# Performance work log

Hardware: AMD Instinct MI355X
Metric: run time of the kernel (lower is better)

## Reference

```python
import jax, jax.numpy as jnp
import numpy as np

N_NODES = 100000
N_EDGES = 1600000
N_GRAPHS = 2048
BN_EPS = 1e-5


def _bn(h, gamma, beta):
    # BatchNorm1d in training mode: biased batch stats over the node axis
    mean = jnp.mean(h, axis=0)
    var = jnp.var(h, axis=0)
    return gamma * (h - mean) * jax.lax.rsqrt(var + BN_EPS) + beta


def _gin_layer(x, src, dst, w1, b1, gamma, beta, w2, b2):
    # GINConv with eps=0: mlp(x + sum_{j->i} x_j)
    agg = jax.ops.segment_sum(x[src], dst, num_segments=N_NODES)
    h = agg + x
    h = h @ w1 + b1
    h = jax.nn.relu(_bn(h, gamma, beta))
    h = h @ w2 + b2
    return jax.nn.relu(h)  # outer F.relu after GINConv (dropout = identity in eval)


def setup_inputs() -> dict:
    key = jax.random.key(0)
    ks = jax.random.split(key, 24)
    d = {}
    d['x'] = jax.random.normal(ks[0], (N_NODES, 66), dtype=jnp.float32)
    d['edge_index'] = jax.random.randint(ks[1], (2, N_EDGES), 0, N_NODES, dtype=jnp.int64)
    d['batch'] = jnp.sort(jax.random.randint(ks[2], (N_NODES,), 0, N_GRAPHS, dtype=jnp.int64))
    dims = [(66, 128), (128, 256), (256, 128)]
    ki = 3
    for li, (din, dout) in enumerate(dims):
        s1 = 1.0 / np.sqrt(din)
        s2 = 1.0 / np.sqrt(dout)
        d[f'g{li}_w1'] = jax.random.uniform(ks[ki + 0], (din, dout), jnp.float32, -s1, s1)
        d[f'g{li}_b1'] = jax.random.uniform(ks[ki + 1], (dout,), jnp.float32, -s1, s1)
        d[f'g{li}_gamma'] = jnp.ones((dout,), jnp.float32)
        d[f'g{li}_beta'] = jnp.zeros((dout,), jnp.float32)
        d[f'g{li}_w2'] = jax.random.uniform(ks[ki + 2], (dout, dout), jnp.float32, -s2, s2)
        d[f'g{li}_b2'] = jax.random.uniform(ks[ki + 3], (dout,), jnp.float32, -s2, s2)
        ki += 4
    fcd = [(128, 1024), (1024, 128)]
    for li, (din, dout) in enumerate(fcd):
        s = 1.0 / np.sqrt(din)
        d[f'fc{li}_w'] = jax.random.uniform(ks[ki + 0], (din, dout), jnp.float32, -s, s)
        d[f'fc{li}_b'] = jax.random.uniform(ks[ki + 1], (dout,), jnp.float32, -s, s)
        ki += 2
    return d


def reference(x, edge_index, batch,
              g0_w1, g0_b1, g0_gamma, g0_beta, g0_w2, g0_b2,
              g1_w1, g1_b1, g1_gamma, g1_beta, g1_w2, g1_b2,
              g2_w1, g2_b1, g2_gamma, g2_beta, g2_w2, g2_b2,
              fc0_w, fc0_b, fc1_w, fc1_b):
    src, dst = edge_index[0], edge_index[1]
    h = _gin_layer(x, src, dst, g0_w1, g0_b1, g0_gamma, g0_beta, g0_w2, g0_b2)
    h = _gin_layer(h, src, dst, g1_w1, g1_b1, g1_gamma, g1_beta, g1_w2, g1_b2)
    h = _gin_layer(h, src, dst, g2_w1, g2_b1, g2_gamma, g2_beta, g2_w2, g2_b2)
    # global_add_pool over graphs
    g = jax.ops.segment_sum(h, batch, num_segments=N_GRAPHS)
    g = jax.nn.relu(g @ fc0_w + fc0_b)
    return g @ fc1_w + fc1_b
```

## Files before the change

### kernel.cpp

```cpp
#include <hip/hip_runtime.h>

#define NNODES 100000
#define NEDGES 1600000
#define NGRAPHS 2048
#define BN_EPS 1e-5f

typedef __attribute__((ext_vector_type(8))) short bf16x8;
typedef __attribute__((ext_vector_type(4))) float f32x4;

__device__ __forceinline__ short f2bf(float x) {
    unsigned u = __float_as_uint(x);
    unsigned r = u + 0x7FFF + ((u >> 16) & 1);
    return (short)(r >> 16);
}
__device__ __forceinline__ float bf2f(short h) {
    return __uint_as_float(((unsigned)(unsigned short)h) << 16);
}

__global__ __launch_bounds__(256) void degoff_kernel(const int* __restrict__ dstA,
                                                     int* __restrict__ degp,
                                                     int* __restrict__ off) {
    int e = blockIdx.x * 256 + threadIdx.x;
    if (e < NEDGES) {
        int d = dstA[e];
        int c = atomicAdd(&degp[d << 4], 1);
        off[e] = (d << 8) | c;
    }
}

__global__ __launch_bounds__(256) void scan1_kernel(const int* __restrict__ degp,
                                                    int* __restrict__ partials) {
    int b = blockIdx.x;
    int i = b * 256 + threadIdx.x;
    int v = (i < NNODES) ? degp[i << 4] : 0;
    __shared__ int wsum[4];
#pragma unroll
    for (int off = 32; off; off >>= 1) v += __shfl_down(v, off);
    if ((threadIdx.x & 63) == 0) wsum[threadIdx.x >> 6] = v;
    __syncthreads();
    if (threadIdx.x == 0) partials[b] = wsum[0] + wsum[1] + wsum[2] + wsum[3];
}

__global__ __launch_bounds__(512) void scan2_kernel(int* __restrict__ partials, int nb) {
    __shared__ int s[512];
    int t = threadIdx.x;
    int v = (t < nb) ? partials[t] : 0;
    s[t] = v;
    __syncthreads();
    for (int off = 1; off < 512; off <<= 1) {
        int u = (t >= off) ? s[t - off] : 0;
        __syncthreads();
        s[t] += u;
        __syncthreads();
    }
    if (t < nb) partials[t] = s[t] - v;
}

__global__ __launch_bounds__(256) void scan3_kernel(const int* __restrict__ degp,
                                                    const int* __restrict__ partials,
                                                    int* __restrict__ rowptr,
                                                    const int* __restrict__ batch,
                                                    int* __restrict__ gstart) {
    int b = blockIdx.x;
    int t = threadIdx.x;
    int i = b * 256 + t;
    __shared__ int s[256];
    int v = (i < NNODES) ? degp[i << 4] : 0;
    s[t] = v;
    __syncthreads();
    for (int off = 1; off < 256; off <<= 1) {
        int u = (t >= off) ? s[t - off] : 0;
        __syncthreads();
        s[t] += u;
        __syncthreads();
    }
    if (i < NNODES) {
        int ex = partials[b] + s[t] - v;
        rowptr[i] = ex;
        int bb = batch[i];
        int bp = (i == 0) ? -1 : batch[i - 1];
        for (int g = bp + 1; g <= bb; ++g) gstart[g] = i;
        if (i == NNODES - 1)
            for (int g = bb + 1; g <= NGRAPHS; ++g) gstart[g] = NNODES;
    }
    if (b == 0 && t == 0) rowptr[NNODES] = NEDGES;
}

__global__ __launch_bounds__(256) void fill2_kernel(const int* __restrict__ srcA,
                                                    const int* __restrict__ rowptr,
                                                    const int* __restrict__ off,
                                                    int* __restrict__ adj) {
    int e = blockIdx.x * 256 + threadIdx.x;
    if (e < NEDGES) {
        int v = off[e];
        adj[rowptr[v >> 8] + (v & 255)] = srcA[e];
    }
}

template <int DIM, int CHUNK, int OSTRIDE, bool SPLIT>
__global__ __launch_bounds__(256) void gather_kernel(const float* __restrict__ x,
                                                     const int* __restrict__ rowptr,
                                                     const int* __restrict__ adj,
                                                     float* __restrict__ agg,
                                                     short* __restrict__ oh,
                                                     short* __restrict__ ol,
                                                     const float* __restrict__ bias) {
    constexpr int PE = DIM / CHUNK;
    constexpr int PEL = SPLIT ? (OSTRIDE / CHUNK) : PE;
    int gid = blockIdx.x * 256 + threadIdx.x;
    if (gid >= NNODES * PEL) return;
    int node = gid / PEL;
    int c = gid - node * PEL;
    if constexpr (SPLIT) {
        if (c >= PE) {
            size_t o = (size_t)node * OSTRIDE + c * CHUNK;
            if constexpr (CHUNK == 4) {
                short4 z;
                z.x = z.y = z.z = z.w = 0;
                *(short4*)&oh[o] = z;
                *(short4*)&ol[o] = z;
            } else {
                short2 z;
                z.x = z.y = 0;
                *(short2*)&oh[o] = z;
                *(short2*)&ol[o] = z;
            }
            return;
        }
    }
    const int beg = rowptr[node];
    const int end = rowptr[node + 1];
    if constexpr (CHUNK == 4) {
        const float4* xp = (const float4*)x;
        float4 acc = xp[(size_t)node * PE + c];
        float4 acc1 = make_float4(0.f, 0.f, 0.f, 0.f);
        int i = beg;
        for (; i + 4 <= end; i += 4) {
            int s0 = adj[i + 0];
            int s1 = adj[i + 1];
            int s2 = adj[i + 2];
            int s3 = adj[i + 3];
            float4 v0 = xp[(size_t)s0 * PE + c];
            float4 v1 = xp[(size_t)s1 * PE + c];
            float4 v2 = xp[(size_t)s2 * PE + c];
            float4 v3 = xp[(size_t)s3 * PE + c];
            acc.x += v0.x + v1.x;
            acc.y += v0.y + v1.y;
            acc.z += v0.z + v1.z;
            acc.w += v0.w + v1.w;
            acc1.x += v2.x + v3.x;
            acc1.y += v2.y + v3.y;
            acc1.z += v2.z + v3.z;
            acc1.w += v2.w + v3.w;
        }
        for (; i < end; ++i) {
            int s = adj[i];
            float4 v = xp[(size_t)s * PE + c];
            acc.x += v.x;
            acc.y += v.y;
            acc.z += v.z;
            acc.w += v.w;
        }
        acc.x += acc1.x;
        acc.y += acc1.y;
        acc.z += acc1.z;
        acc.w += acc1.w;
        if (bias) {
            float4 b = *(const float4*)&bias[c * 4];
            acc.x += b.x;
            acc.y += b.y;
            acc.z += b.z;
            acc.w += b.w;
        }
        if constexpr (SPLIT) {
            size_t o = (size_t)node * OSTRIDE + c * 4;
            short4 h4, l4;
            h4.x = f2bf(acc.x);
            l4.x = f2bf(acc.x - bf2f(h4.x));
            h4.y = f2bf(acc.y);
            l4.y = f2bf(acc.y - bf2f(h4.y));
            h4.z = f2bf(acc.z);
            l4.z = f2bf(acc.z - bf2f(h4.z));
            h4.w = f2bf(acc.w);
            l4.w = f2bf(acc.w - bf2f(h4.w));
            *(short4*)&oh[o] = h4;
            *(short4*)&ol[o] = l4;
        } else {
            *(float4*)&agg[(size_t)node * OSTRIDE + c * 4] = acc;
        }
    } else {
        const float2* xp = (const float2*)x;
        float2 acc = xp[(size_t)node * PE + c];
        float2 acc1 = make_float2(0.f, 0.f);
        int i = beg;
        for (; i + 4 <= end; i += 4) {
            int s0 = adj[i + 0];
            int s1 = adj[i + 1];
            int s2 = adj[i + 2];
            int s3 = adj[i + 3];
            float2 v0 = xp[(size_t)s0 * PE + c];
            float2 v1 = xp[(size_t)s1 * PE + c];
            float2 v2 = xp[(size_t)s2 * PE + c];
            float2 v3 = xp[(size_t)s3 * PE + c];
            acc.x += v0.x + v1.x;
            acc.y += v0.y + v1.y;
            acc1.x += v2.x + v3.x;
            acc1.y += v2.y + v3.y;
        }
        for (; i < end; ++i) {
            int s = adj[i];
            float2 v = xp[(size_t)s * PE + c];
            acc.x += v.x;
            acc.y += v.y;
        }
        acc.x += acc1.x;
        acc.y += acc1.y;
        if constexpr (SPLIT) {
            size_t o = (size_t)node * OSTRIDE + c * 2;
            short2 h2, l2;
            h2.x = f2bf(acc.x);
            l2.x = f2bf(acc.x - bf2f(h2.x));
            h2.y = f2bf(acc.y);
            l2.y = f2bf(acc.y - bf2f(h2.y));
            *(short2*)&oh[o] = h2;
            *(short2*)&ol[o] = l2;
        } else {
            *(float2*)&agg[(size_t)node * OSTRIDE + c * 2] = acc;
        }
    }
}

template <int N>
__global__ __launch_bounds__(256) void bnstats_kernel(const float* __restrict__ h,
                                                      float* __restrict__ sums) {
    constexpr int SHIFT = (N == 128) ? 7 : 8;
    int t = blockIdx.x * 256 + threadIdx.x;
    int col = t & (N - 1);
    int slice = t >> SHIFT;
    float s = 0.f, s2 = 0.f;
    for (int r = slice; r < NNODES; r += 256) {
        float v = h[(size_t)r * N + col];
        s += v;
        s2 += v * v;
    }
    atomicAdd(&sums[col], s);
    atomicAdd(&sums[256 + col], s2);
}

__global__ void bnfinal_kernel(float* __restrict__ sums, const float* __restrict__ gamma,
                               const float* __restrict__ beta, float* __restrict__ scsh, int N,
                               float invM) {
    int c = threadIdx.x;
    if (c < N) {
        float mean = sums[c] * invM;
        float var = sums[256 + c] * invM - mean * mean;
        float sc = gamma[c] * rsqrtf(var + BN_EPS);
        scsh[c] = sc;
        scsh[256 + c] = beta[c] - mean * sc;
    }
    sums[c] = 0.f;
    sums[256 + c] = 0.f;
}

struct WDesc {
    const float* W;
    int Kw, N, KT, hioff, looff;
};
struct WDescs {
    WDesc d[8];
    int cum[9];
};
__global__ __launch_bounds__(256) void wprep_all_kernel(WDescs wd, short* __restrict__ wf) {
    int idx = blockIdx.x * 256 + threadIdx.x;
    if (idx >= wd.cum[8]) return;
    int s = 0;
#pragma unroll
    for (int i = 1; i < 8; ++i) s += (idx >= wd.cum[i]);
    int r = idx - wd.cum[s];
    const WDesc D = wd.d[s];
    int j = r & 7;
    int lane = (r >> 3) & 63;
    int t = r >> 9;
    int kt = t % D.KT;
    int nt = t / D.KT;
    int k = kt * 32 + ((lane >> 4) << 3) + j;
    int n = (nt << 4) + (lane & 15);
    float w = (k < D.Kw) ? D.W[(size_t)k * D.N + n] : 0.f;
    short hi = f2bf(w);
    wf[D.hioff + r] = hi;
    wf[D.looff + r] = f2bf(w - bf2f(hi));
}

template <int NT, int KTLOOP, bool BNRELU_A, bool RELU_OUT, bool FUSE_STATS, bool SPLITK,
          bool ASPLIT, bool SPLIT_OUT, int MINW>
__global__ __launch_bounds__(256, MINW) void gemm_mfma_kernel(
    const float* __restrict__ A, const short* __restrict__ Ah, const short* __restrict__ Al,
    const short* __restrict__ whi, const short* __restrict__ wlo, const float* __restrict__ bias,
    const float* __restrict__ scsh, float* __restrict__ C, short* __restrict__ Ch,
    short* __restrict__ Cl, float* __restrict__ stats, int M, int Kst, int KT, int N) {
    __shared__ float sstat[512];
    const int tid = threadIdx.x;
    const int wave = tid >> 6;
    const int lane = tid & 63;
    const int quad = lane >> 4;
    const int l16 = lane & 15;
    const int mrow = blockIdx.x * 64 + wave * 16 + l16;
    const int ngrp = blockIdx.y * NT * 16;
    const size_t wgrp = (size_t)blockIdx.y * NT * KT * 512;
    const int ktbeg = SPLITK ? blockIdx.z * KTLOOP : 0;
    float* Cb = SPLITK ? C + (size_t)blockIdx.z * M * N : C;

    if (FUSE_STATS) {
        sstat[tid] = 0.f;
        sstat[tid + 256] = 0.f;
        __syncthreads();
    }

    f32x4 acc[NT] = {};

    auto kstep = [&](int kt) {
        const int kq = kt * 32 + quad * 8;
        bf16x8 ahi, alo;
        if constexpr (ASPLIT) {
            ahi = *(const bf16x8*)(Ah + (size_t)mrow * Kst + kq);
            alo = *(const bf16x8*)(Al + (size_t)mrow * Kst + kq);
        } else {
            const float* ap = A + (size_t)mrow * Kst + kq;
            float4 x0 = *(const float4*)ap;
            float4 x1 = *(const float4*)(ap + 4);
            float a8[8] = {x0.x, x0.y, x0.z, x0.w, x1.x, x1.y, x1.z, x1.w};
            if constexpr (BNRELU_A) {
                float4 sc0 = *(const float4*)&scsh[kq];
                float4 sc1 = *(const float4*)&scsh[kq + 4];
                float4 sh0 = *(const float4*)&scsh[256 + kq];
                float4 sh1 = *(const float4*)&scsh[256 + kq + 4];
                float sc[8] = {sc0.x, sc0.y, sc0.z, sc0.w, sc1.x, sc1.y, sc1.z, sc1.w};
                float sh[8] = {sh0.x, sh0.y, sh0.z, sh0.w, sh1.x, sh1.y, sh1.z, sh1.w};
#pragma unroll
                for (int i = 0; i < 8; ++i) a8[i] = fmaxf(a8[i] * sc[i] + sh[i], 0.f);
            }
#pragma unroll
            for (int i = 0; i < 8; ++i) {
                short h = f2bf(a8[i]);
                ahi[i] = h;
                alo[i] = f2bf(a8[i] - bf2f(h));
            }
        }
#pragma unroll
        for (int nt = 0; nt < NT; ++nt) {
            const size_t boff = wgrp + (((size_t)nt * KT + kt) << 9) + ((size_t)lane << 3);
            bf16x8 bh = *(const bf16x8*)(whi + boff);
            bf16x8 bl = *(const bf16x8*)(wlo + boff);
            acc[nt] = __builtin_amdgcn_mfma_f32_16x16x32_bf16(ahi, bh, acc[nt], 0, 0, 0);
            acc[nt] = __builtin_amdgcn_mfma_f32_16x16x32_bf16(alo, bh, acc[nt], 0, 0, 0);
            acc[nt] = __builtin_amdgcn_mfma_f32_16x16x32_bf16(ahi, bl, acc[nt], 0, 0, 0);
            acc[nt] = __builtin_amdgcn_mfma_f32_16x16x32_bf16(alo, bl, acc[nt], 0, 0, 0);
        }
    };

    if constexpr (ASPLIT) {
#pragma unroll 2
        for (int k = 0; k < KTLOOP; ++k) kstep(ktbeg + k);
    } else {
#pragma unroll 1
        for (int k = 0; k < KTLOOP; ++k) kstep(ktbeg + k);
    }

    const int mbase = blockIdx.x * 64 + wave * 16 + quad * 4;
#pragma unroll
    for (int nt = 0; nt < NT; ++nt) {
        int gn = ngrp + nt * 16 + l16;
        float bv = bias ? bias[gn] : 0.f;
        float s = 0.f, s2 = 0.f;
#pragma unroll
        for (int r = 0; r < 4; ++r) {
            int gm = mbase + r;
            float v = acc[nt][r] + bv;
            if (RELU_OUT) v = fmaxf(v, 0.f);
            if (gm < M) {
                if constexpr (SPLIT_OUT) {
                    short h = f2bf(v);
                    Ch[(size_t)gm * N + gn] = h;
                    Cl[(size_t)gm * N + gn] = f2bf(v - bf2f(h));
                } else {
                    Cb[(size_t)gm * N + gn] = v;
                }
                if (FUSE_STATS) {
                    s += v;
                    s2 += v * v;
                }
            }
        }
        if (FUSE_STATS) {
            s += __shfl_xor(s, 16);
            s += __shfl_xor(s, 32);
            s2 += __shfl_xor(s2, 16);
            s2 += __shfl_xor(s2, 32);
            if (quad == 0) {
                atomicAdd(&sstat[gn], s);
                atomicAdd(&sstat[256 + gn], s2);
            }
        }
    }
    if (FUSE_STATS) {
        __syncthreads();
        if (tid < N) {
            atomicAdd(&stats[tid], sstat[tid]);
            atomicAdd(&stats[256 + tid], sstat[256 + tid]);
        }
    }
}

__global__ __launch_bounds__(256) void splitk_reduce_kernel(const float* __restrict__ part,
                                                            const float* __restrict__ bias,
                                                            float* __restrict__ out) {
    const int i4 = blockIdx.x * 256 + threadIdx.x;
    const int TOT4 = NGRAPHS * 128 / 4;
    if (i4 >= TOT4) return;
    const float4* p = (const float4*)part;
    float4 acc = make_float4(0.f, 0.f, 0.f, 0.f);
#pragma unroll
    for (int c = 0; c < 8; ++c) {
        float4 v = p[(size_t)c * TOT4 + i4];
        acc.x += v.x;
        acc.y += v.y;
        acc.z += v.z;
        acc.w += v.w;
    }
    float4 b = ((const float4*)bias)[i4 & 31];
    acc.x += b.x;
    acc.y += b.y;
    acc.z += b.z;
    acc.w += b.w;
    ((float4*)out)[i4] = acc;
}

template <bool SPLIT>
__global__ __launch_bounds__(128) void pool_seg_kernel(const float* __restrict__ h,
                                                       const int* __restrict__ gstart,
                                                       float* __restrict__ g,
                                                       short* __restrict__ oh,
                                                       short* __restrict__ ol) {
    int gr = blockIdx.x;
    int t = threadIdx.x;
    int beg = gstart[gr];
    int end = gstart[gr + 1];
    float acc = 0.f;
    for (int r = beg; r < end; ++r) acc += h[(size_t)r * 128 + t];
    if constexpr (SPLIT) {
        short hh = f2bf(acc);
        oh[(size_t)gr * 128 + t] = hh;
        ol[(size_t)gr * 128 + t] = f2bf(acc - bf2f(hh));
    } else {
        g[(size_t)gr * 128 + t] = acc;
    }
}

extern "C" void kernel_launch(void* const* d_in, const int* in_sizes, int n_in, void* d_out,
                              int out_size, void* d_ws, size_t ws_size, hipStream_t stream) {
    const float* x = (const float*)d_in[0];
    const int* ei = (const int*)d_in[1];
    const int* batch = (const int*)d_in[2];
    const int* srcA = ei;
    const int* dstA = ei + NEDGES;

    const float* g0_w1 = (const float*)d_in[3];
    const float* g0_b1 = (const float*)d_in[4];
    const float* g0_ga = (const float*)d_in[5];
    const float* g0_be = (const float*)d_in[6];
    const float* g0_w2 = (const float*)d_in[7];
    const float* g0_b2 = (const float*)d_in[8];
    const float* g1_w1 = (const float*)d_in[9];
    const float* g1_b1 = (const float*)d_in[10];
    const float* g1_ga = (const float*)d_in[11];
    const float* g1_be = (const float*)d_in[12];
    const float* g1_w2 = (const float*)d_in[13];
    const float* g1_b2 = (const float*)d_in[14];
    const float* g2_w1 = (const float*)d_in[15];
    const float* g2_b1 = (const float*)d_in[16];
    const float* g2_ga = (const float*)d_in[17];
    const float* g2_be = (const float*)d_in[18];
    const float* g2_w2 = (const float*)d_in[19];
    const float* g2_b2 = (const float*)d_in[20];
    const float* fc0_w = (const float*)d_in[21];
    const float* fc0_b = (const float*)d_in[22];
    const float* fc1_w = (const float*)d_in[23];
    const float* fc1_b = (const float*)d_in[24];

    float* ws = (float*)d_ws;
    const size_t BUF = (size_t)NNODES * 256;
    float* R0 = ws;
    float* R1 = R0 + BUF;
    float* stats = R1 + BUF;
    float* scsh = stats + 512;
    float* g = scsh + 512;
    float* gh = g + (size_t)NGRAPHS * 128;
    int* rowptr = (int*)(gh + (size_t)NGRAPHS * 1024);
    int* adj = rowptr + NNODES + 4;
    int* partials = adj + NEDGES;
    int* gstart = partials + 512;
    short* wf = (short*)(gstart + 2052);

    int* degp = (int*)R0;
    int* off = degp + NNODES * 16;

    short* whi[8];
    short* wlo[8];
    for (int i = 0; i < 6; ++i) {
        whi[i] = wf + (size_t)i * 131072;
        wlo[i] = whi[i] + 65536;
    }
    whi[6] = wf + 6 * 131072;
    wlo[6] = whi[6] + 131072;
    whi[7] = whi[6] + 262144;
    wlo[7] = whi[7] + 131072;

    short* P0h = (short*)R0;
    short* P0l = P0h + (size_t)NNODES * 96;
    short* P1h = (short*)R1;
    short* P1l = P1h + (size_t)NNODES * 128;
    short* P2h = (short*)R1;
    short* P2l = P2h + (size_t)NNODES * 256;
    short* GPh = (short*)g;
    short* GPl = GPh + (size_t)NGRAPHS * 128;
    short* GHh = (short*)gh;
    short* GHl = GHh + (size_t)NGRAPHS * 1024;

    const int GB = (NNODES + 63) / 64;
    const int NB = (NNODES + 255) / 256;
    const int EB = (NEDGES + 255) / 256;

    hipMemsetAsync(degp, 0, (size_t)NNODES * 16 * sizeof(int), stream);
    hipMemsetAsync(stats, 0, 512 * sizeof(float), stream);
    degoff_kernel<<<EB, 256, 0, stream>>>(dstA, degp, off);
    scan1_kernel<<<NB, 256, 0, stream>>>(degp, partials);
    scan2_kernel<<<1, 512, 0, stream>>>(partials, NB);
    scan3_kernel<<<NB, 256, 0, stream>>>(degp, partials, rowptr, batch, gstart);
    fill2_kernel<<<EB, 256, 0, stream>>>(srcA, rowptr, off, adj);

    {
        WDescs wd;
        const float* Wp[8] = {g0_w1, g0_w2, g1_w1, g1_w2, g2_w1, g2_w2, fc0_w, fc1_w};
        const int Kw[8] = {66, 128, 128, 256, 256, 128, 128, 1024};
        const int Nn[8] = {128, 128, 256, 256, 128, 128, 1024, 128};
        const int KT[8] = {3, 4, 4, 8, 8, 4, 4, 32};
        int cum = 0;
        wd.cum[0] = 0;
        for (int i = 0; i < 8; ++i) {
            wd.d[i].W = Wp[i];
            wd.d[i].Kw = Kw[i];
            wd.d[i].N = Nn[i];
            wd.d[i].KT = KT[i];
            wd.d[i].hioff = (int)(whi[i] - wf);
            wd.d[i].looff = (int)(wlo[i] - wf);
            cum += (Nn[i] >> 4) * KT[i] * 512;
            wd.cum[i + 1] = cum;
        }
        wprep_all_kernel<<<(wd.cum[8] + 255) / 256, 256, 0, stream>>>(wd, wf);
    }

    gather_kernel<66, 2, 96, true><<<(NNODES * 48 + 255) / 256, 256, 0, stream>>>(
        x, rowptr, adj, nullptr, P0h, P0l, nullptr);
    gemm_mfma_kernel<8, 3, false, false, true, false, true, false, 4><<<GB, 256, 0, stream>>>(
        nullptr, P0h, P0l, whi[0], wlo[0], g0_b1, nullptr, R1, nullptr, nullptr, stats, NNODES, 96,
        3, 128);
    bnfinal_kernel<<<1, 256, 0, stream>>>(stats, g0_ga, g0_be, scsh, 128, 1.0f / NNODES);
    gemm_mfma_kernel<8, 4, true, true, false, false, false, false, 4><<<GB, 256, 0, stream>>>(
        R1, nullptr, nullptr, whi[1], wlo[1], g0_b2, scsh, R0, nullptr, nullptr, nullptr, NNODES,
        128, 4, 128);

    gather_kernel<128, 4, 128, true><<<(NNODES * 32 + 255) / 256, 256, 0, stream>>>(
        R0, rowptr, adj, nullptr, P1h, P1l, nullptr);
    gemm_mfma_kernel<16, 4, false, false, true, false, true, false, 3><<<GB, 256, 0, stream>>>(
        nullptr, P1h, P1l, whi[2], wlo[2], g1_b1, nullptr, R0, nullptr, nullptr, stats, NNODES,
        128, 4, 256);
    bnfinal_kernel<<<1, 256, 0, stream>>>(stats, g1_ga, g1_be, scsh, 256, 1.0f / NNODES);
    gemm_mfma_kernel<8, 8, true, true, false, false, false, true, 4>
        <<<dim3(GB, 2), 256, 0, stream>>>(R0, nullptr, nullptr, whi[3], wlo[3], g1_b2, scsh,
                                          nullptr, P2h, P2l, nullptr, NNODES, 256, 8, 256);

    gemm_mfma_kernel<8, 8, false, false, false, false, true, false, 4><<<GB, 256, 0, stream>>>(
        nullptr, P2h, P2l, whi[4], wlo[4], nullptr, nullptr, R0, nullptr, nullptr, nullptr, NNODES,
        256, 8, 128);
    gather_kernel<128, 4, 128, false><<<(NNODES * 32 + 255) / 256, 256, 0, stream>>>(
        R0, rowptr, adj, R1, nullptr, nullptr, g2_b1);
    bnstats_kernel<128><<<128, 256, 0, stream>>>(R1, stats);
    bnfinal_kernel<<<1, 256, 0, stream>>>(stats, g2_ga, g2_be, scsh, 128, 1.0f / NNODES);
    gemm_mfma_kernel<8, 4, true, true, false, false, false, false, 4><<<GB, 256, 0, stream>>>(
        R1, nullptr, nullptr, whi[5], wlo[5], g2_b2, scsh, R0, nullptr, nullptr, nullptr, NNODES,
        128, 4, 128);

    pool_seg_kernel<true><<<NGRAPHS, 128, 0, stream>>>(R0, gstart, nullptr, GPh, GPl);

    gemm_mfma_kernel<8, 4, false, true, false, false, true, true, 4>
        <<<dim3(NGRAPHS / 64, 8), 256, 0, stream>>>(nullptr, GPh, GPl, whi[6], wlo[6], fc0_b,
                                                    nullptr, nullptr, GHh, GHl, nullptr, NGRAPHS,
                                                    128, 4, 1024);
    gemm_mfma_kernel<8, 4, false, false, false, true, true, false, 4>
        <<<dim3(NGRAPHS / 64, 1, 8), 256, 0, stream>>>(nullptr, GHh, GHl, whi[7], wlo[7], nullptr,
                                                       nullptr, R1, nullptr, nullptr, nullptr,
                                                       NGRAPHS, 1024, 32, 128);
    splitk_reduce_kernel<<<(NGRAPHS * 128 / 4 + 255) / 256, 256, 0, stream>>>(R1, fc1_b,
                                                                              (float*)d_out);
}
```

Before: 1.161 ms.

## Software-pipeline GEMM B/A loads, unroll gather by 8, split layer-1 GEMM over N

The MFMA GEMM becomes a fully unrolled software pipeline. Weight fragments are prefetched several steps ahead in a register ring, and A fragments (including the BN+ReLU bf16 split) are loaded and converted one k-step early into double buffers. KT becomes a template parameter so these offsets are compile-time constants. The gather loop is unrolled to 8 neighbors to keep more loads in flight, and the 256-wide layer-1 GEMM now uses NT=8 with a 2-way grid split instead of NT=16. The deeper prefetch raises register pressure and could lower occupancy.

```diff
diff --git a/kernel.cpp b/kernel.cpp
--- a/kernel.cpp
+++ b/kernel.cpp
@@ -135,54 +135,48 @@
         float4 acc = xp[(size_t)node * PE + c];
         float4 acc1 = make_float4(0.f, 0.f, 0.f, 0.f);
         int i = beg;
-        for (; i + 4 <= end; i += 4) {
-            int s0 = adj[i + 0];
-            int s1 = adj[i + 1];
-            int s2 = adj[i + 2];
-            int s3 = adj[i + 3];
+        for (; i + 8 <= end; i += 8) {
+            int s0 = adj[i + 0], s1 = adj[i + 1], s2 = adj[i + 2], s3 = adj[i + 3];
+            int s4 = adj[i + 4], s5 = adj[i + 5], s6 = adj[i + 6], s7 = adj[i + 7];
             float4 v0 = xp[(size_t)s0 * PE + c];
             float4 v1 = xp[(size_t)s1 * PE + c];
             float4 v2 = xp[(size_t)s2 * PE + c];
             float4 v3 = xp[(size_t)s3 * PE + c];
-            acc.x += v0.x + v1.x;
-            acc.y += v0.y + v1.y;
-            acc.z += v0.z + v1.z;
-            acc.w += v0.w + v1.w;
-            acc1.x += v2.x + v3.x;
-            acc1.y += v2.y + v3.y;
-            acc1.z += v2.z + v3.z;
-            acc1.w += v2.w + v3.w;
+            float4 v4 = xp[(size_t)s4 * PE + c];
+            float4 v5 = xp[(size_t)s5 * PE + c];
+            float4 v6 = xp[(size_t)s6 * PE + c];
+            float4 v7 = xp[(size_t)s7 * PE + c];
+            acc.x += v0.x + v1.x; acc.y += v0.y + v1.y; acc.z += v0.z + v1.z; acc.w += v0.w + v1.w;
+            acc1.x += v2.x + v3.x; acc1.y += v2.y + v3.y; acc1.z += v2.z + v3.z; acc1.w += v2.w + v3.w;
+            acc.x += v4.x + v5.x; acc.y += v4.y + v5.y; acc.z += v4.z + v5.z; acc.w += v4.w + v5.w;
+            acc1.x += v6.x + v7.x; acc1.y += v6.y + v7.y; acc1.z += v6.z + v7.z; acc1.w += v6.w + v7.w;
+        }
+        for (; i + 4 <= end; i += 4) {
+            int s0 = adj[i + 0], s1 = adj[i + 1], s2 = adj[i + 2], s3 = adj[i + 3];
+            float4 v0 = xp[(size_t)s0 * PE + c];
+            float4 v1 = xp[(size_t)s1 * PE + c];
+            float4 v2 = xp[(size_t)s2 * PE + c];
+            float4 v3 = xp[(size_t)s3 * PE + c];
+            acc.x += v0.x + v1.x; acc.y += v0.y + v1.y; acc.z += v0.z + v1.z; acc.w += v0.w + v1.w;
+            acc1.x += v2.x + v3.x; acc1.y += v2.y + v3.y; acc1.z += v2.z + v3.z; acc1.w += v2.w + v3.w;
         }
         for (; i < end; ++i) {
             int s = adj[i];
             float4 v = xp[(size_t)s * PE + c];
-            acc.x += v.x;
-            acc.y += v.y;
-            acc.z += v.z;
-            acc.w += v.w;
-        }
-        acc.x += acc1.x;
-        acc.y += acc1.y;
-        acc.z += acc1.z;
-        acc.w += acc1.w;
+            acc.x += v.x; acc.y += v.y; acc.z += v.z; acc.w += v.w;
+        }
+        acc.x += acc1.x; acc.y += acc1.y; acc.z += acc1.z; acc.w += acc1.w;
         if (bias) {
             float4 b = *(const float4*)&bias[c * 4];
-            acc.x += b.x;
-            acc.y += b.y;
-            acc.z += b.z;
-            acc.w += b.w;
+            acc.x += b.x; acc.y += b.y; acc.z += b.z; acc.w += b.w;
         }
         if constexpr (SPLIT) {
             size_t o = (size_t)node * OSTRIDE + c * 4;
             short4 h4, l4;
-            h4.x = f2bf(acc.x);
-            l4.x = f2bf(acc.x - bf2f(h4.x));
-            h4.y = f2bf(acc.y);
-            l4.y = f2bf(acc.y - bf2f(h4.y));
-            h4.z = f2bf(acc.z);
-            l4.z = f2bf(acc.z - bf2f(h4.z));
-            h4.w = f2bf(acc.w);
-            l4.w = f2bf(acc.w - bf2f(h4.w));
+            h4.x = f2bf(acc.x); l4.x = f2bf(acc.x - bf2f(h4.x));
+            h4.y = f2bf(acc.y); l4.y = f2bf(acc.y - bf2f(h4.y));
+            h4.z = f2bf(acc.z); l4.z = f2bf(acc.z - bf2f(h4.z));
+            h4.w = f2bf(acc.w); l4.w = f2bf(acc.w - bf2f(h4.w));
             *(short4*)&oh[o] = h4;
             *(short4*)&ol[o] = l4;
         } else {
@@ -193,35 +187,42 @@
         float2 acc = xp[(size_t)node * PE + c];
         float2 acc1 = make_float2(0.f, 0.f);
         int i = beg;
-        for (; i + 4 <= end; i += 4) {
-            int s0 = adj[i + 0];
-            int s1 = adj[i + 1];
-            int s2 = adj[i + 2];
-            int s3 = adj[i + 3];
+        for (; i + 8 <= end; i += 8) {
+            int s0 = adj[i + 0], s1 = adj[i + 1], s2 = adj[i + 2], s3 = adj[i + 3];
+            int s4 = adj[i + 4], s5 = adj[i + 5], s6 = adj[i + 6], s7 = adj[i + 7];
             float2 v0 = xp[(size_t)s0 * PE + c];
             float2 v1 = xp[(size_t)s1 * PE + c];
             float2 v2 = xp[(size_t)s2 * PE + c];
             float2 v3 = xp[(size_t)s3 * PE + c];
-            acc.x += v0.x + v1.x;
-            acc.y += v0.y + v1.y;
-            acc1.x += v2.x + v3.x;
-            acc1.y += v2.y + v3.y;
+            float2 v4 = xp[(size_t)s4 * PE + c];
+            float2 v5 = xp[(size_t)s5 * PE + c];
+            float2 v6 = xp[(size_t)s6 * PE + c];
+            float2 v7 = xp[(size_t)s7 * PE + c];
+            acc.x += v0.x + v1.x; acc.y += v0.y + v1.y;
+            acc1.x += v2.x + v3.x; acc1.y += v2.y + v3.y;
+            acc.x += v4.x + v5.x; acc.y += v4.y + v5.y;
+            acc1.x += v6.x + v7.x; acc1.y += v6.y + v7.y;
+        }
+        for (; i + 4 <= end; i += 4) {
+            int s0 = adj[i + 0], s1 = adj[i + 1], s2 = adj[i + 2], s3 = adj[i + 3];
+            float2 v0 = xp[(size_t)s0 * PE + c];
+            float2 v1 = xp[(size_t)s1 * PE + c];
+            float2 v2 = xp[(size_t)s2 * PE + c];
+            float2 v3 = xp[(size_t)s3 * PE + c];
+            acc.x += v0.x + v1.x; acc.y += v0.y + v1.y;
+            acc1.x += v2.x + v3.x; acc1.y += v2.y + v3.y;
         }
         for (; i < end; ++i) {
             int s = adj[i];
             float2 v = xp[(size_t)s * PE + c];
-            acc.x += v.x;
-            acc.y += v.y;
-        }
-        acc.x += acc1.x;
-        acc.y += acc1.y;
+            acc.x += v.x; acc.y += v.y;
+        }
+        acc.x += acc1.x; acc.y += acc1.y;
         if constexpr (SPLIT) {
             size_t o = (size_t)node * OSTRIDE + c * 2;
             short2 h2, l2;
-            h2.x = f2bf(acc.x);
-            l2.x = f2bf(acc.x - bf2f(h2.x));
-            h2.y = f2bf(acc.y);
-            l2.y = f2bf(acc.y - bf2f(h2.y));
+            h2.x = f2bf(acc.x); l2.x = f2bf(acc.x - bf2f(h2.x));
+            h2.y = f2bf(acc.y); l2.y = f2bf(acc.y - bf2f(h2.y));
             *(short2*)&oh[o] = h2;
             *(short2*)&ol[o] = l2;
         } else {
@@ -291,13 +292,37 @@
     wf[D.looff + r] = f2bf(w - bf2f(hi));
 }
 
-template <int NT, int KTLOOP, bool BNRELU_A, bool RELU_OUT, bool FUSE_STATS, bool SPLITK,
+#define GEMM_CONVA(DK, SLOT)                                                        \
+    {                                                                               \
+        float a8_[8];                                                               \
+        _Pragma("unroll") for (int i_ = 0; i_ < 8; ++i_) a8_[i_] = rawA[i_];        \
+        if constexpr (BNRELU_A) {                                                   \
+            const int kq_ = (ktbeg + (DK)) * 32 + quad * 8;                         \
+            float4 sc0_ = *(const float4*)&scsh[kq_];                               \
+            float4 sc1_ = *(const float4*)&scsh[kq_ + 4];                           \
+            float4 sh0_ = *(const float4*)&scsh[256 + kq_];                         \
+            float4 sh1_ = *(const float4*)&scsh[256 + kq_ + 4];                     \
+            float sc_[8] = {sc0_.x, sc0_.y, sc0_.z, sc0_.w,                         \
+                            sc1_.x, sc1_.y, sc1_.z, sc1_.w};                        \
+            float sh_[8] = {sh0_.x, sh0_.y, sh0_.z, sh0_.w,                         \
+                            sh1_.x, sh1_.y, sh1_.z, sh1_.w};                        \
+            _Pragma("unroll") for (int i_ = 0; i_ < 8; ++i_)                        \
+                a8_[i_] = fmaxf(a8_[i_] * sc_[i_] + sh_[i_], 0.f);                  \
+        }                                                                           \
+        _Pragma("unroll") for (int i_ = 0; i_ < 8; ++i_) {                          \
+            short h_ = f2bf(a8_[i_]);                                               \
+            ahr[SLOT][i_] = h_;                                                     \
+            alr[SLOT][i_] = f2bf(a8_[i_] - bf2f(h_));                               \
+        }                                                                           \
+    }
+
+template <int NT, int KTLOOP, int KTT, bool BNRELU_A, bool RELU_OUT, bool FUSE_STATS, bool SPLITK,
           bool ASPLIT, bool SPLIT_OUT, int MINW>
 __global__ __launch_bounds__(256, MINW) void gemm_mfma_kernel(
     const float* __restrict__ A, const short* __restrict__ Ah, const short* __restrict__ Al,
     const short* __restrict__ whi, const short* __restrict__ wlo, const float* __restrict__ bias,
     const float* __restrict__ scsh, float* __restrict__ C, short* __restrict__ Ch,
-    short* __restrict__ Cl, float* __restrict__ stats, int M, int Kst, int KT, int N) {
+    short* __restrict__ Cl, float* __restrict__ stats, int M, int Kst, int N) {
     __shared__ float sstat[512];
     const int tid = threadIdx.x;
     const int wave = tid >> 6;
@@ -306,7 +331,7 @@
     const int l16 = lane & 15;
     const int mrow = blockIdx.x * 64 + wave * 16 + l16;
     const int ngrp = blockIdx.y * NT * 16;
-    const size_t wgrp = (size_t)blockIdx.y * NT * KT * 512;
+    const size_t wgrp = (size_t)blockIdx.y * NT * KTT * 512;
     const int ktbeg = SPLITK ? blockIdx.z * KTLOOP : 0;
     float* Cb = SPLITK ? C + (size_t)blockIdx.z * M * N : C;
 
@@ -316,54 +341,71 @@
         __syncthreads();
     }
 
+    const short* Bh0 = whi + wgrp + ((size_t)ktbeg << 9) + ((size_t)lane << 3);
+    const short* Bl0 = wlo + wgrp + ((size_t)ktbeg << 9) + ((size_t)lane << 3);
+    const short* Abh = nullptr;
+    const short* Abl = nullptr;
+    const float* Abase = nullptr;
+    if constexpr (ASPLIT) {
+        Abh = Ah + (size_t)mrow * Kst + ktbeg * 32 + quad * 8;
+        Abl = Al + (size_t)mrow * Kst + ktbeg * 32 + quad * 8;
+    } else {
+        Abase = A + (size_t)mrow * Kst + ktbeg * 32 + quad * 8;
+    }
+
+    constexpr int S = KTLOOP * NT;
+    constexpr int D0 = ASPLIT ? 4 : 3;
+    constexpr int DD = (D0 < S) ? D0 : S;
+
     f32x4 acc[NT] = {};
-
-    auto kstep = [&](int kt) {
-        const int kq = kt * 32 + quad * 8;
-        bf16x8 ahi, alo;
+    bf16x8 bhq[DD], blq[DD];
+    bf16x8 ahr[2], alr[2];
+    float rawA[8];
+
+    if constexpr (ASPLIT) {
+        ahr[0] = *(const bf16x8*)(Abh);
+        alr[0] = *(const bf16x8*)(Abl);
+    } else {
+        *(float4*)&rawA[0] = *(const float4*)(Abase);
+        *(float4*)&rawA[4] = *(const float4*)(Abase + 4);
+        GEMM_CONVA(0, 0);
+    }
+#pragma unroll
+    for (int d = 0; d < DD; ++d) {
+        const int pkt = d / NT, pnt = d % NT;
+        bhq[d] = *(const bf16x8*)(Bh0 + (size_t)((pnt * KTT + pkt) << 9));
+        blq[d] = *(const bf16x8*)(Bl0 + (size_t)((pnt * KTT + pkt) << 9));
+    }
+
+#pragma unroll
+    for (int s = 0; s < S; ++s) {
+        const int kt = s / NT;
+        const int nt = s % NT;
+        const int slot = s % DD;
+        const int pa = kt & 1;
+        acc[nt] = __builtin_amdgcn_mfma_f32_16x16x32_bf16(ahr[pa], bhq[slot], acc[nt], 0, 0, 0);
+        acc[nt] = __builtin_amdgcn_mfma_f32_16x16x32_bf16(alr[pa], bhq[slot], acc[nt], 0, 0, 0);
+        acc[nt] = __builtin_amdgcn_mfma_f32_16x16x32_bf16(ahr[pa], blq[slot], acc[nt], 0, 0, 0);
+        acc[nt] = __builtin_amdgcn_mfma_f32_16x16x32_bf16(alr[pa], blq[slot], acc[nt], 0, 0, 0);
+        if (s + DD < S) {
+            const int fkt = (s + DD) / NT, fnt = (s + DD) % NT;
+            bhq[slot] = *(const bf16x8*)(Bh0 + (size_t)((fnt * KTT + fkt) << 9));
+            blq[slot] = *(const bf16x8*)(Bl0 + (size_t)((fnt * KTT + fkt) << 9));
+        }
         if constexpr (ASPLIT) {
-            ahi = *(const bf16x8*)(Ah + (size_t)mrow * Kst + kq);
-            alo = *(const bf16x8*)(Al + (size_t)mrow * Kst + kq);
+            if (nt == 0 && kt + 1 < KTLOOP) {
+                ahr[(kt + 1) & 1] = *(const bf16x8*)(Abh + (kt + 1) * 32);
+                alr[(kt + 1) & 1] = *(const bf16x8*)(Abl + (kt + 1) * 32);
+            }
         } else {
-            const float* ap = A + (size_t)mrow * Kst + kq;
-            float4 x0 = *(const float4*)ap;
-            float4 x1 = *(const float4*)(ap + 4);
-            float a8[8] = {x0.x, x0.y, x0.z, x0.w, x1.x, x1.y, x1.z, x1.w};
-            if constexpr (BNRELU_A) {
-                float4 sc0 = *(const float4*)&scsh[kq];
-                float4 sc1 = *(const float4*)&scsh[kq + 4];
-                float4 sh0 = *(const float4*)&scsh[256 + kq];
-                float4 sh1 = *(const float4*)&scsh[256 + kq + 4];
-                float sc[8] = {sc0.x, sc0.y, sc0.z, sc0.w, sc1.x, sc1.y, sc1.z, sc1.w};
-                float sh[8] = {sh0.x, sh0.y, sh0.z, sh0.w, sh1.x, sh1.y, sh1.z, sh1.w};
-#pragma unroll
-                for (int i = 0; i < 8; ++i) a8[i] = fmaxf(a8[i] * sc[i] + sh[i], 0.f);
+            if (nt == 0 && kt + 1 < KTLOOP) {
+                *(float4*)&rawA[0] = *(const float4*)(Abase + (kt + 1) * 32);
+                *(float4*)&rawA[4] = *(const float4*)(Abase + (kt + 1) * 32 + 4);
             }
-#pragma unroll
-            for (int i = 0; i < 8; ++i) {
-                short h = f2bf(a8[i]);
-                ahi[i] = h;
-                alo[i] = f2bf(a8[i] - bf2f(h));
+            if (nt == (NT >= 3 ? NT - 2 : 0) && kt + 1 < KTLOOP) {
+                GEMM_CONVA(kt + 1, (kt + 1) & 1);
             }
         }
-#pragma unroll
-        for (int nt = 0; nt < NT; ++nt) {
-            const size_t boff = wgrp + (((size_t)nt * KT + kt) << 9) + ((size_t)lane << 3);
-            bf16x8 bh = *(const bf16x8*)(whi + boff);
-            bf16x8 bl = *(const bf16x8*)(wlo + boff);
-            acc[nt] = __builtin_amdgcn_mfma_f32_16x16x32_bf16(ahi, bh, acc[nt], 0, 0, 0);
-            acc[nt] = __builtin_amdgcn_mfma_f32_16x16x32_bf16(alo, bh, acc[nt], 0, 0, 0);
-            acc[nt] = __builtin_amdgcn_mfma_f32_16x16x32_bf16(ahi, bl, acc[nt], 0, 0, 0);
-            acc[nt] = __builtin_amdgcn_mfma_f32_16x16x32_bf16(alo, bl, acc[nt], 0, 0, 0);
-        }
-    };
-
-    if constexpr (ASPLIT) {
-#pragma unroll 2
-        for (int k = 0; k < KTLOOP; ++k) kstep(ktbeg + k);
-    } else {
-#pragma unroll 1
-        for (int k = 0; k < KTLOOP; ++k) kstep(ktbeg + k);
     }
 
     const int mbase = blockIdx.x * 64 + wave * 16 + quad * 4;
@@ -561,45 +603,45 @@
 
     gather_kernel<66, 2, 96, true><<<(NNODES * 48 + 255) / 256, 256, 0, stream>>>(
         x, rowptr, adj, nullptr, P0h, P0l, nullptr);
-    gemm_mfma_kernel<8, 3, false, false, true, false, true, false, 4><<<GB, 256, 0, stream>>>(
+    gemm_mfma_kernel<8, 3, 3, false, false, true, false, true, false, 4><<<GB, 256, 0, stream>>>(
         nullptr, P0h, P0l, whi[0], wlo[0], g0_b1, nullptr, R1, nullptr, nullptr, stats, NNODES, 96,
-        3, 128);
+        128);
     bnfinal_kernel<<<1, 256, 0, stream>>>(stats, g0_ga, g0_be, scsh, 128, 1.0f / NNODES);
-    gemm_mfma_kernel<8, 4, true, true, false, false, false, false, 4><<<GB, 256, 0, stream>>>(
+    gemm_mfma_kernel<8, 4, 4, true, true, false, false, false, false, 4><<<GB, 256, 0, stream>>>(
         R1, nullptr, nullptr, whi[1], wlo[1], g0_b2, scsh, R0, nullptr, nullptr, nullptr, NNODES,
-        128, 4, 128);
+        128, 128);
 
     gather_kernel<128, 4, 128, true><<<(NNODES * 32 + 255) / 256, 256, 0, stream>>>(
         R0, rowptr, adj, nullptr, P1h, P1l, nullptr);
-    gemm_mfma_kernel<16, 4, false, false, true, false, true, false, 3><<<GB, 256, 0, stream>>>(
-        nullptr, P1h, P1l, whi[2], wlo[2], g1_b1, nullptr, R0, nullptr, nullptr, stats, NNODES,
-        128, 4, 256);
+    gemm_mfma_kernel<8, 4, 4, false, false, true, false, true, false, 4>
+        <<<dim3(GB, 2), 256, 0, stream>>>(nullptr, P1h, P1l, whi[2], wlo[2], g1_b1, nullptr, R0,
+                                          nullptr, nullptr, stats, NNODES, 128, 256);
     bnfinal_kernel<<<1, 256, 0, stream>>>(stats, g1_ga, g1_be, scsh, 256, 1.0f / NNODES);
-    gemm_mfma_kernel<8, 8, true, true, false, false, false, true, 4>
+    gemm_mfma_kernel<8, 8, 8, true, true, false, false, false, true, 4>
         <<<dim3(GB, 2), 256, 0, stream>>>(R0, nullptr, nullptr, whi[3], wlo[3], g1_b2, scsh,
-                                          nullptr, P2h, P2l, nullptr, NNODES, 256, 8, 256);
-
-    gemm_mfma_kernel<8, 8, false, false, false, false, true, false, 4><<<GB, 256, 0, stream>>>(
+                                          nullptr, P2h, P2l, nullptr, NNODES, 256, 256);
+
+    gemm_mfma_kernel<8, 8, 8, false, false, false, false, true, false, 4><<<GB, 256, 0, stream>>>(
         nullptr, P2h, P2l, whi[4], wlo[4], nullptr, nullptr, R0, nullptr, nullptr, nullptr, NNODES,
-        256, 8, 128);
+        256, 128);
     gather_kernel<128, 4, 128, false><<<(NNODES * 32 + 255) / 256, 256, 0, stream>>>(
         R0, rowptr, adj, R1, nullptr, nullptr, g2_b1);
     bnstats_kernel<128><<<128, 256, 0, stream>>>(R1, stats);
     bnfinal_kernel<<<1, 256, 0, stream>>>(stats, g2_ga, g2_be, scsh, 128, 1.0f / NNODES);
-    gemm_mfma_kernel<8, 4, true, true, false, false, false, false, 4><<<GB, 256, 0, stream>>>(
+    gemm_mfma_kernel<8, 4, 4, true, true, false, false, false, false, 4><<<GB, 256, 0, stream>>>(
         R1, nullptr, nullptr, whi[5], wlo[5], g2_b2, scsh, R0, nullptr, nullptr, nullptr, NNODES,
-        128, 4, 128);
+        128, 128);
 
     pool_seg_kernel<true><<<NGRAPHS, 128, 0, stream>>>(R0, gstart, nullptr, GPh, GPl);
 
-    gemm_mfma_kernel<8, 4, false, true, false, false, true, true, 4>
+    gemm_mfma_kernel<8, 4, 4, false, true, false, false, true, true, 4>
         <<<dim3(NGRAPHS / 64, 8), 256, 0, stream>>>(nullptr, GPh, GPl, whi[6], wlo[6], fc0_b,
                                                     nullptr, nullptr, GHh, GHl, nullptr, NGRAPHS,
-                                                    128, 4, 1024);
-    gemm_mfma_kernel<8, 4, false, false, false, true, true, false, 4>
+                                                    128, 1024);
+    gemm_mfma_kernel<8, 4, 32, false, false, false, true, true, false, 4>
         <<<dim3(NGRAPHS / 64, 1, 8), 256, 0, stream>>>(nullptr, GHh, GHl, whi[7], wlo[7], nullptr,
                                                        nullptr, R1, nullptr, nullptr, nullptr,
-                                                       NGRAPHS, 1024, 32, 128);
+                                                       NGRAPHS, 1024, 128);
     splitk_reduce_kernel<<<(NGRAPHS * 128 / 4 + 255) / 256, 256, 0, stream>>>(R1, fc1_b,
                                                                               (float*)d_out);
 }
```

New measurement: 4.103 ms. +253.5%, slower.
